# Kernel tuning notes

Measured on AMD Instinct MI355X. Metric: run time of the kernel, lower is better.

## Reference

```python
import jax, jax.numpy as jnp
import numpy as np

LEAKY_RELU_SLOPE = 0.2
N = 8192
F = 256


def setup_inputs() -> dict:
    key = jax.random.key(0)
    k1, k2, k3 = jax.random.split(key, 3)
    h = jax.random.normal(k1, (N, F), dtype=jnp.float32)
    # sparse-ish adjacency with guaranteed self-loops so no row is all -inf
    adjacency = jax.random.bernoulli(k2, 0.05, (N, N))
    adjacency = adjacency.at[jnp.arange(N), jnp.arange(N)].set(True)
    # xavier_uniform for a: shape (F, 2), gain=1 -> limit = sqrt(6/(F+2))
    limit = float(np.sqrt(6.0 / (F + 2)))
    a = jax.random.uniform(k3, (F, 2), minval=-limit, maxval=limit, dtype=jnp.float32)
    return {"h": h, "adjacency": adjacency, "a": a}


def reference(h, adjacency, a):
    e = h @ a                      # [N, 2]
    e1 = e[:, 0:1]                 # [N, 1]
    e2 = e[:, 1:2]                 # [N, 1]
    scores = e1 + e2.T             # [N, N] broadcast
    scores = jnp.where(scores >= 0, scores, LEAKY_RELU_SLOPE * scores)
    scores = jnp.where(adjacency, scores, -jnp.inf)
    return jax.nn.softmax(scores, axis=1)
```

## Files before the change

kernel.cpp:

```cpp
#include <hip/hip_runtime.h>

#define GN 8192
#define GF 256
#define SLOPE 0.2f

typedef int   vint4   __attribute__((ext_vector_type(4)));
typedef float vfloat4 __attribute__((ext_vector_type(4)));

__global__ __launch_bounds__(256) void compute_e_kernel(
        const float* __restrict__ h, const float* __restrict__ a,
        float* __restrict__ e1, float* __restrict__ e2) {
    int wave = threadIdx.x >> 6;
    int lane = threadIdx.x & 63;
    int row  = blockIdx.x * 4 + wave;

    const float4* h4 = (const float4*)(h + (size_t)row * GF);
    float4 hv = h4[lane];
    const float4* a4 = (const float4*)a;
    float4 av0 = a4[2 * lane];
    float4 av1 = a4[2 * lane + 1];

    float d1 = hv.x * av0.x + hv.y * av0.z + hv.z * av1.x + hv.w * av1.z;
    float d2 = hv.x * av0.y + hv.y * av0.w + hv.z * av1.y + hv.w * av1.w;
    #pragma unroll
    for (int off = 32; off; off >>= 1) {
        d1 += __shfl_xor(d1, off);
        d2 += __shfl_xor(d2, off);
    }
    if (lane == 0) {
        e1[row] = d1;
        e2[row] = d2;
    }
}

template <int MODE>
__device__ __forceinline__ void attn_row_body(
        const void* __restrict__ adjv,
        const float* __restrict__ e1, const float* __restrict__ e2,
        float* __restrict__ out, float* __restrict__ wsum) {
    const int row = blockIdx.x;
    const int tid = threadIdx.x;
    const float se1 = e1[row];
    const size_t rowbase = (size_t)row * GN;
    const size_t vecbase = (size_t)row * 2048;

    const float4* e2v = (const float4*)e2;

    float v[16];
    float acc = 0.f;

    #pragma unroll
    for (int c = 0; c < 4; ++c) {
        const int j4 = c * 512 + tid;
        float4 ev = e2v[j4];
        bool m0, m1, m2, m3;
        if (MODE == 0) {
            vint4 aw = __builtin_nontemporal_load(&((const vint4*)adjv)[vecbase + j4]);
            m0 = aw.x != 0; m1 = aw.y != 0; m2 = aw.z != 0; m3 = aw.w != 0;
        } else if (MODE == 1) {
            unsigned int aw = __builtin_nontemporal_load(&((const unsigned int*)adjv)[vecbase + j4]);
            m0 = (aw & 0x000000FFu) != 0; m1 = (aw & 0x0000FF00u) != 0;
            m2 = (aw & 0x00FF0000u) != 0; m3 = (aw & 0xFF000000u) != 0;
        } else {
            vfloat4 aw = __builtin_nontemporal_load(&((const vfloat4*)adjv)[vecbase + j4]);
            m0 = aw.x != 0.f; m1 = aw.y != 0.f; m2 = aw.z != 0.f; m3 = aw.w != 0.f;
        }
        float s0 = se1 + ev.x; s0 = s0 >= 0.f ? s0 : SLOPE * s0;
        float s1 = se1 + ev.y; s1 = s1 >= 0.f ? s1 : SLOPE * s1;
        float s2 = se1 + ev.z; s2 = s2 >= 0.f ? s2 : SLOPE * s2;
        float s3 = se1 + ev.w; s3 = s3 >= 0.f ? s3 : SLOPE * s3;
        float x0 = m0 ? __expf(s0) : 0.f;
        float x1 = m1 ? __expf(s1) : 0.f;
        float x2 = m2 ? __expf(s2) : 0.f;
        float x3 = m3 ? __expf(s3) : 0.f;
        v[c * 4 + 0] = x0; v[c * 4 + 1] = x1;
        v[c * 4 + 2] = x2; v[c * 4 + 3] = x3;
        acc += x0 + x1 + x2 + x3;
    }

    #pragma unroll
    for (int off = 32; off; off >>= 1) acc += __shfl_xor(acc, off);
    if ((tid & 63) == 0) wsum[tid >> 6] = acc;
    __syncthreads();
    float total = 0.f;
    #pragma unroll
    for (int w = 0; w < 8; ++w) total += wsum[w];
    const float inv = 1.0f / total;

    vfloat4* out4 = (vfloat4*)(out + rowbase);
    #pragma unroll
    for (int c = 0; c < 4; ++c) {
        vfloat4 o;
        o.x = v[c * 4 + 0] * inv; o.y = v[c * 4 + 1] * inv;
        o.z = v[c * 4 + 2] * inv; o.w = v[c * 4 + 3] * inv;
        __builtin_nontemporal_store(o, &out4[c * 512 + tid]);
    }
}

__global__ __launch_bounds__(512) void attn_row_kernel(
        const void* __restrict__ adjv,
        const float* __restrict__ e1, const float* __restrict__ e2,
        float* __restrict__ out) {
    __shared__ int s_flags;
    __shared__ float wsum[8];
    const int tid = threadIdx.x;
    if (tid == 0) s_flags = 0;
    __syncthreads();

    uint4 hw = ((const uint4*)adjv)[tid];
    int f = 0;
    {
        unsigned int w;
        w = hw.x; if (w == 0x3F800000u) f |= 2; else if (w > 1u && (w & 0xFEFEFEFEu) == 0u) f |= 1;
        w = hw.y; if (w == 0x3F800000u) f |= 2; else if (w > 1u && (w & 0xFEFEFEFEu) == 0u) f |= 1;
        w = hw.z; if (w == 0x3F800000u) f |= 2; else if (w > 1u && (w & 0xFEFEFEFEu) == 0u) f |= 1;
        w = hw.w; if (w == 0x3F800000u) f |= 2; else if (w > 1u && (w & 0xFEFEFEFEu) == 0u) f |= 1;
    }
    if (f) atomicOr(&s_flags, f);
    __syncthreads();
    const int mode = (s_flags & 1) ? 1 : ((s_flags & 2) ? 2 : 0);

    if (mode == 0)      attn_row_body<0>(adjv, e1, e2, out, wsum);
    else if (mode == 1) attn_row_body<1>(adjv, e1, e2, out, wsum);
    else                attn_row_body<2>(adjv, e1, e2, out, wsum);
}

extern "C" void kernel_launch(void* const* d_in, const int* in_sizes, int n_in,
                              void* d_out, int out_size, void* d_ws, size_t ws_size,
                              hipStream_t stream) {
    const float* h   = (const float*)d_in[0];
    const void*  adj = (const void*)d_in[1];
    const float* a   = (const float*)d_in[2];
    float* out = (float*)d_out;

    float* e1 = (float*)d_ws;
    float* e2 = e1 + GN;

    compute_e_kernel<<<GN / 4, 256, 0, stream>>>(h, a, e1, e2);
    attn_row_kernel<<<GN, 512, 0, stream>>>(adj, e1, e2, out);
}
```

Measured before the change: 437.7 us.

## Hoist adjacency dtype detection into e-kernel and use branchless mask multiply

Adjacency format detection moves out of every attention block and into block 0 of the e-computation kernel, which stores the mode in workspace, so each of the 8192 row blocks no longer loads a sample, runs an atomic and hits two barriers. The mask is also applied by converting adjacency values to float and multiplying them into exp(score), and leaky ReLU is computed with fmaxf, replacing the selects. The multiply assumes adjacency values are exactly 0 or 1; any other nonzero value would scale the output.

```diff
diff --git a/kernel.cpp b/kernel.cpp
--- a/kernel.cpp
+++ b/kernel.cpp
@@ -9,7 +9,25 @@
 
 __global__ __launch_bounds__(256) void compute_e_kernel(
         const float* __restrict__ h, const float* __restrict__ a,
-        float* __restrict__ e1, float* __restrict__ e2) {
+        const unsigned int* __restrict__ adjw,
+        float* __restrict__ e1, float* __restrict__ e2,
+        int* __restrict__ mode) {
+    if (blockIdx.x == 0) {
+        __shared__ int s_flags;
+        if (threadIdx.x == 0) s_flags = 0;
+        __syncthreads();
+        int f = 0;
+        for (int i = threadIdx.x; i < 2048; i += 256) {
+            unsigned int w = adjw[i];
+            if (w == 0x3F800000u) f |= 2;
+            else if (w > 1u && (w & 0xFEFEFEFEu) == 0u) f |= 1;
+        }
+        if (f) atomicOr(&s_flags, f);
+        __syncthreads();
+        if (threadIdx.x == 0)
+            *mode = (s_flags & 1) ? 1 : ((s_flags & 2) ? 2 : 0);
+    }
+
     int wave = threadIdx.x >> 6;
     int lane = threadIdx.x & 63;
     int row  = blockIdx.x * 4 + wave;
@@ -53,29 +71,31 @@
     for (int c = 0; c < 4; ++c) {
         const int j4 = c * 512 + tid;
         float4 ev = e2v[j4];
-        bool m0, m1, m2, m3;
+        float m0, m1, m2, m3;
         if (MODE == 0) {
             vint4 aw = __builtin_nontemporal_load(&((const vint4*)adjv)[vecbase + j4]);
-            m0 = aw.x != 0; m1 = aw.y != 0; m2 = aw.z != 0; m3 = aw.w != 0;
+            m0 = (float)aw.x; m1 = (float)aw.y; m2 = (float)aw.z; m3 = (float)aw.w;
         } else if (MODE == 1) {
             unsigned int aw = __builtin_nontemporal_load(&((const unsigned int*)adjv)[vecbase + j4]);
-            m0 = (aw & 0x000000FFu) != 0; m1 = (aw & 0x0000FF00u) != 0;
-            m2 = (aw & 0x00FF0000u) != 0; m3 = (aw & 0xFF000000u) != 0;
+            m0 = (float)(aw & 0xFFu);
+            m1 = (float)((aw >> 8) & 0xFFu);
+            m2 = (float)((aw >> 16) & 0xFFu);
+            m3 = (float)(aw >> 24);
         } else {
             vfloat4 aw = __builtin_nontemporal_load(&((const vfloat4*)adjv)[vecbase + j4]);
-            m0 = aw.x != 0.f; m1 = aw.y != 0.f; m2 = aw.z != 0.f; m3 = aw.w != 0.f;
+            m0 = aw.x; m1 = aw.y; m2 = aw.z; m3 = aw.w;
         }
-        float s0 = se1 + ev.x; s0 = s0 >= 0.f ? s0 : SLOPE * s0;
-        float s1 = se1 + ev.y; s1 = s1 >= 0.f ? s1 : SLOPE * s1;
-        float s2 = se1 + ev.z; s2 = s2 >= 0.f ? s2 : SLOPE * s2;
-        float s3 = se1 + ev.w; s3 = s3 >= 0.f ? s3 : SLOPE * s3;
-        float x0 = m0 ? __expf(s0) : 0.f;
-        float x1 = m1 ? __expf(s1) : 0.f;
-        float x2 = m2 ? __expf(s2) : 0.f;
-        float x3 = m3 ? __expf(s3) : 0.f;
+        float s0 = se1 + ev.x; s0 = fmaxf(s0, SLOPE * s0);
+        float s1 = se1 + ev.y; s1 = fmaxf(s1, SLOPE * s1);
+        float s2 = se1 + ev.z; s2 = fmaxf(s2, SLOPE * s2);
+        float s3 = se1 + ev.w; s3 = fmaxf(s3, SLOPE * s3);
+        float x0 = __expf(s0) * m0;
+        float x1 = __expf(s1) * m1;
+        float x2 = __expf(s2) * m2;
+        float x3 = __expf(s3) * m3;
         v[c * 4 + 0] = x0; v[c * 4 + 1] = x1;
         v[c * 4 + 2] = x2; v[c * 4 + 3] = x3;
-        acc += x0 + x1 + x2 + x3;
+        acc += (x0 + x1) + (x2 + x3);
     }
 
     #pragma unroll
@@ -98,31 +118,14 @@
 }
 
 __global__ __launch_bounds__(512) void attn_row_kernel(
-        const void* __restrict__ adjv,
+        const int* __restrict__ mode, const void* __restrict__ adjv,
         const float* __restrict__ e1, const float* __restrict__ e2,
         float* __restrict__ out) {
-    __shared__ int s_flags;
     __shared__ float wsum[8];
-    const int tid = threadIdx.x;
-    if (tid == 0) s_flags = 0;
-    __syncthreads();
-
-    uint4 hw = ((const uint4*)adjv)[tid];
-    int f = 0;
-    {
-        unsigned int w;
-        w = hw.x; if (w == 0x3F800000u) f |= 2; else if (w > 1u && (w & 0xFEFEFEFEu) == 0u) f |= 1;
-        w = hw.y; if (w == 0x3F800000u) f |= 2; else if (w > 1u && (w & 0xFEFEFEFEu) == 0u) f |= 1;
-        w = hw.z; if (w == 0x3F800000u) f |= 2; else if (w > 1u && (w & 0xFEFEFEFEu) == 0u) f |= 1;
-        w = hw.w; if (w == 0x3F800000u) f |= 2; else if (w > 1u && (w & 0xFEFEFEFEu) == 0u) f |= 1;
-    }
-    if (f) atomicOr(&s_flags, f);
-    __syncthreads();
-    const int mode = (s_flags & 1) ? 1 : ((s_flags & 2) ? 2 : 0);
-
-    if (mode == 0)      attn_row_body<0>(adjv, e1, e2, out, wsum);
-    else if (mode == 1) attn_row_body<1>(adjv, e1, e2, out, wsum);
-    else                attn_row_body<2>(adjv, e1, e2, out, wsum);
+    const int m = *mode;
+    if (m == 0)      attn_row_body<0>(adjv, e1, e2, out, wsum);
+    else if (m == 1) attn_row_body<1>(adjv, e1, e2, out, wsum);
+    else             attn_row_body<2>(adjv, e1, e2, out, wsum);
 }
 
 extern "C" void kernel_launch(void* const* d_in, const int* in_sizes, int n_in,
@@ -133,9 +136,11 @@
     const float* a   = (const float*)d_in[2];
     float* out = (float*)d_out;
 
-    float* e1 = (float*)d_ws;
-    float* e2 = e1 + GN;
+    float* e1   = (float*)d_ws;
+    float* e2   = e1 + GN;
+    int*   mode = (int*)(e2 + GN);
 
-    compute_e_kernel<<<GN / 4, 256, 0, stream>>>(h, a, e1, e2);
-    attn_row_kernel<<<GN, 512, 0, stream>>>(adj, e1, e2, out);
+    compute_e_kernel<<<GN / 4, 256, 0, stream>>>(h, a, (const unsigned int*)adj,
+                                                 e1, e2, mode);
+    attn_row_kernel<<<GN, 512, 0, stream>>>(mode, adj, e1, e2, out);
 }
```

Result: faster. 427.3 us (-2.4%).
